# Performance work log

Measured on AMD Instinct MI355X. Metric: run time of the kernel, lower is better.

## Reference

```python
import jax, jax.numpy as jnp
import numpy as np

B, C, P, H, W = 64, 2048, 4, 14, 14
HID = C * P // 2  # 4096
S = H * W         # 196


def setup_inputs() -> dict:
    key = jax.random.key(0)
    k1, k2, k3, k4, k5 = jax.random.split(key, 5)
    x = jax.random.normal(k1, (B, C, H, W), dtype=jnp.float32)
    w1 = jax.random.normal(k2, (HID, C), dtype=jnp.float32) * 0.02
    b1 = jnp.zeros((HID,), dtype=jnp.float32)
    w2 = jax.random.normal(k3, (C * P, HID), dtype=jnp.float32) * 0.02
    b2 = jnp.zeros((C * P,), dtype=jnp.float32)
    return {"x": x, "w1": w1, "b1": b1, "w2": w2, "b2": b2}


def reference(x, w1, b1, w2, b2):
    # SE-style gating: global average pool -> fc1 -> sigmoid -> fc2 -> sigmoid
    g = x.mean(axis=(2, 3))                                  # [B, C]
    h = jax.nn.sigmoid(g @ w1.T + b1)                        # [B, HID]
    w = jax.nn.sigmoid(h @ w2.T + b2).reshape(B, P, C)       # grouping_result [B, P, C]
    # Weighted feature: mean over channels of w[b,p,c] * x[b,c,s].
    # Original materializes [B,P,C,196] then AdaptiveAvgPool3d over C;
    # mathematically this is a batched matmul divided by C.
    xs = x.reshape(B, C, S)                                  # [B, C, 196]
    feat = jnp.einsum('bpc,bcs->bps', w, xs) / C             # [B, P, 196]
    return (w, feat.reshape(B, P, H, W))
```

## Files before the change

kernel.cpp:

```cpp
#include <hip/hip_runtime.h>
#include <cstdint>
#include <cstddef>

typedef __attribute__((ext_vector_type(4))) float  f32x4;
typedef __attribute__((ext_vector_type(8))) short  short8;

__device__ __forceinline__ short f2bf(float f) {
  unsigned u = __float_as_uint(f);
  u += 0x7FFF + ((u >> 16) & 1);
  return (short)(u >> 16);
}
__device__ __forceinline__ float sigmoidf(float x) {
  return 1.0f / (1.0f + __expf(-x));
}

__global__ __launch_bounds__(256) void pool_kernel(const float* __restrict__ x,
                                                   short* __restrict__ g) {
  __shared__ float sums[784];
  const int tid = threadIdx.x;
  const f32x4* base = (const f32x4*)(x + (size_t)blockIdx.x * (16 * 196));
#pragma unroll
  for (int it = 0; it < 4; ++it) {
    int i = it * 256 + tid;
    if (it < 3 || tid < 16) {
      f32x4 v = base[i];
      sums[i] = v[0] + v[1] + v[2] + v[3];
    }
  }
  __syncthreads();
  if (tid < 16) {
    float s = 0.f;
#pragma unroll
    for (int j = 0; j < 49; ++j) s += sums[tid * 49 + j];
    g[blockIdx.x * 16 + tid] = f2bf(s * (1.0f / 196.0f));
  }
}

template<int N, int K, int WAVES, bool OUT_BF16, bool ZERO_FEAT>
__device__ __forceinline__ void gemm_body(const short* __restrict__ A,
                                          const float* __restrict__ B,
                                          const float* __restrict__ bias,
                                          void* __restrict__ outp,
                                          float* __restrict__ zbuf,
                                          float* __restrict__ red) {
  constexpr int KW = K / WAVES;
  constexpr int NK = KW / 32;
  constexpr int NT = WAVES * 64;
  const int n0  = blockIdx.x * 16;
  const int tid = threadIdx.x;
  const int l   = tid & 63;
  const int wv  = tid >> 6;
  const int kw0 = wv * KW;

  if constexpr (ZERO_FEAT) {
    if (tid < 98) zbuf[blockIdx.x * 98 + tid] = 0.f;
  }

  const int ko = (l >> 4) * 8;
  const float* Bp = B + (size_t)(n0 + (l & 15)) * K + kw0 + ko;
  const short* Ap = A + (size_t)(l & 15) * K + kw0 + ko;

  f32x4 acc0 = {}, acc1 = {}, acc2 = {}, acc3 = {};

  f32x4 bc0 = *(const f32x4*)(Bp);
  f32x4 bc1 = *(const f32x4*)(Bp + 4);
  short8 ac0 = *(const short8*)(Ap);
  short8 ac1 = *(const short8*)(Ap + 16 * K);
  short8 ac2 = *(const short8*)(Ap + 32 * K);
  short8 ac3 = *(const short8*)(Ap + 48 * K);

  for (int t = 0; t < NK; ++t) {
    f32x4 bn0 = {}, bn1 = {};
    short8 an0 = {}, an1 = {}, an2 = {}, an3 = {};
    if (t + 1 < NK) {
      const float* bp = Bp + (t + 1) * 32;
      const short* ap = Ap + (t + 1) * 32;
      bn0 = *(const f32x4*)(bp);
      bn1 = *(const f32x4*)(bp + 4);
      an0 = *(const short8*)(ap);
      an1 = *(const short8*)(ap + 16 * K);
      an2 = *(const short8*)(ap + 32 * K);
      an3 = *(const short8*)(ap + 48 * K);
    }
    short8 bb;
    bb[0] = f2bf(bc0[0]); bb[1] = f2bf(bc0[1]); bb[2] = f2bf(bc0[2]); bb[3] = f2bf(bc0[3]);
    bb[4] = f2bf(bc1[0]); bb[5] = f2bf(bc1[1]); bb[6] = f2bf(bc1[2]); bb[7] = f2bf(bc1[3]);
    acc0 = __builtin_amdgcn_mfma_f32_16x16x32_bf16(ac0, bb, acc0, 0, 0, 0);
    acc1 = __builtin_amdgcn_mfma_f32_16x16x32_bf16(ac1, bb, acc1, 0, 0, 0);
    acc2 = __builtin_amdgcn_mfma_f32_16x16x32_bf16(ac2, bb, acc2, 0, 0, 0);
    acc3 = __builtin_amdgcn_mfma_f32_16x16x32_bf16(ac3, bb, acc3, 0, 0, 0);
    bc0 = bn0; bc1 = bn1;
    ac0 = an0; ac1 = an1; ac2 = an2; ac3 = an3;
  }

  {
    float* rw = red + wv * 1024;
    const int mb = (l >> 4) << 2;
    const int nn = l & 15;
#pragma unroll
    for (int r = 0; r < 4; ++r) rw[(0  + mb + r) * 16 + nn] = acc0[r];
#pragma unroll
    for (int r = 0; r < 4; ++r) rw[(16 + mb + r) * 16 + nn] = acc1[r];
#pragma unroll
    for (int r = 0; r < 4; ++r) rw[(32 + mb + r) * 16 + nn] = acc2[r];
#pragma unroll
    for (int r = 0; r < 4; ++r) rw[(48 + mb + r) * 16 + nn] = acc3[r];
  }
  __syncthreads();

#pragma unroll
  for (int i = tid; i < 1024; i += NT) {
    float s = 0.f;
#pragma unroll
    for (int w = 0; w < WAVES; ++w) s += red[w * 1024 + i];
    int m  = i >> 4;
    int nn = n0 + (i & 15);
    s = sigmoidf(s + bias[nn]);
    if constexpr (OUT_BF16) ((short*)outp)[(size_t)m * N + nn] = f2bf(s);
    else                    ((float*)outp)[(size_t)m * N + nn] = s;
  }
}

__global__ __launch_bounds__(1024, 4) void gemm1_kernel(const short* __restrict__ A,
                                                        const float* __restrict__ B,
                                                        const float* __restrict__ bias,
                                                        short* __restrict__ outp) {
  __shared__ float red[16 * 1024];
  gemm_body<4096, 2048, 16, true, false>(A, B, bias, outp, nullptr, red);
}

__global__ __launch_bounds__(512, 4) void gemm2_kernel(const short* __restrict__ A,
                                                       const float* __restrict__ B,
                                                       const float* __restrict__ bias,
                                                       float* __restrict__ outp,
                                                       float* __restrict__ zbuf) {
  __shared__ float red[8 * 1024];
  gemm_body<8192, 4096, 8, false, true>(A, B, bias, outp, zbuf, red);
}

__global__ __launch_bounds__(256) void einsum_kernel(const float* __restrict__ x,
                                                     const float* __restrict__ wg,
                                                     float* __restrict__ feat) {
  const int b   = blockIdx.x >> 4;
  const int cc  = blockIdx.x & 15;
  const int tid = threadIdx.x;
  if (tid >= 196) return;
  const float* wp = wg + (size_t)b * 8192 + cc * 128;
  const float* xp = x + (size_t)b * 2048 * 196 + (size_t)cc * 128 * 196 + tid;
  float a0 = 0.f, a1 = 0.f, a2 = 0.f, a3 = 0.f;
#pragma unroll 8
  for (int c = 0; c < 128; ++c) {
    float xv = xp[(size_t)c * 196];
    a0 = __builtin_fmaf(wp[c],        xv, a0);
    a1 = __builtin_fmaf(wp[2048 + c], xv, a1);
    a2 = __builtin_fmaf(wp[4096 + c], xv, a2);
    a3 = __builtin_fmaf(wp[6144 + c], xv, a3);
  }
  const float invC = 1.0f / 2048.0f;
  atomicAdd(feat + (b * 4 + 0) * 196 + tid, a0 * invC);
  atomicAdd(feat + (b * 4 + 1) * 196 + tid, a1 * invC);
  atomicAdd(feat + (b * 4 + 2) * 196 + tid, a2 * invC);
  atomicAdd(feat + (b * 4 + 3) * 196 + tid, a3 * invC);
}

extern "C" void kernel_launch(void* const* d_in, const int* in_sizes, int n_in,
                              void* d_out, int out_size, void* d_ws, size_t ws_size,
                              hipStream_t stream) {
  const float* x  = (const float*)d_in[0];
  const float* w1 = (const float*)d_in[1];
  const float* b1 = (const float*)d_in[2];
  const float* w2 = (const float*)d_in[3];
  const float* b2 = (const float*)d_in[4];
  float* out = (float*)d_out;

  short* g_bf = (short*)d_ws;
  short* h_bf = g_bf + 64 * 2048;

  float* wout = out;
  float* feat = out + 524288;

  pool_kernel<<<8192, 256, 0, stream>>>(x, g_bf);

  gemm1_kernel<<<4096 / 16, 1024, 0, stream>>>(g_bf, w1, b1, h_bf);

  gemm2_kernel<<<8192 / 16, 512, 0, stream>>>(h_bf, w2, b2, wout, feat);

  einsum_kernel<<<64 * 16, 256, 0, stream>>>(x, wout, feat);
}
```

Baseline: 100.4 us.

## Vectorize einsum loads, drop A-prefetch in GEMM, raise gemm2 occupancy bound

The einsum kernel now has 49 threads per block, each loading four contiguous spatial values as a float4 and keeping four-wide accumulators per group. Block size falls from 256 to 64 threads. The GEMM loop no longer software-prefetches the bf16 A operand and instead loads it at the start of each iteration, which frees registers. gemm2's launch bound rises to 6 blocks per CU. f2bf now calls the HIP library conversion. Together these aim to cut per-element load overhead and register pressure, but they risk exposing A-load latency and leaving lanes idle in einsum waves.

```diff
diff --git a/kernel.cpp b/kernel.cpp
--- a/kernel.cpp
+++ b/kernel.cpp
@@ -1,4 +1,5 @@
 #include <hip/hip_runtime.h>
+#include <hip/hip_bf16.h>
 #include <cstdint>
 #include <cstddef>
 
@@ -6,9 +7,8 @@
 typedef __attribute__((ext_vector_type(8))) short  short8;
 
 __device__ __forceinline__ short f2bf(float f) {
-  unsigned u = __float_as_uint(f);
-  u += 0x7FFF + ((u >> 16) & 1);
-  return (short)(u >> 16);
+  __hip_bfloat16 h = __float2bfloat16(f);
+  return *reinterpret_cast<short*>(&h);
 }
 __device__ __forceinline__ float sigmoidf(float x) {
   return 1.0f / (1.0f + __expf(-x));
@@ -64,24 +64,19 @@
 
   f32x4 bc0 = *(const f32x4*)(Bp);
   f32x4 bc1 = *(const f32x4*)(Bp + 4);
-  short8 ac0 = *(const short8*)(Ap);
-  short8 ac1 = *(const short8*)(Ap + 16 * K);
-  short8 ac2 = *(const short8*)(Ap + 32 * K);
-  short8 ac3 = *(const short8*)(Ap + 48 * K);
 
   for (int t = 0; t < NK; ++t) {
     f32x4 bn0 = {}, bn1 = {};
-    short8 an0 = {}, an1 = {}, an2 = {}, an3 = {};
     if (t + 1 < NK) {
       const float* bp = Bp + (t + 1) * 32;
-      const short* ap = Ap + (t + 1) * 32;
       bn0 = *(const f32x4*)(bp);
       bn1 = *(const f32x4*)(bp + 4);
-      an0 = *(const short8*)(ap);
-      an1 = *(const short8*)(ap + 16 * K);
-      an2 = *(const short8*)(ap + 32 * K);
-      an3 = *(const short8*)(ap + 48 * K);
     }
+    const short* ap = Ap + t * 32;
+    short8 ac0 = *(const short8*)(ap);
+    short8 ac1 = *(const short8*)(ap + 16 * K);
+    short8 ac2 = *(const short8*)(ap + 32 * K);
+    short8 ac3 = *(const short8*)(ap + 48 * K);
     short8 bb;
     bb[0] = f2bf(bc0[0]); bb[1] = f2bf(bc0[1]); bb[2] = f2bf(bc0[2]); bb[3] = f2bf(bc0[3]);
     bb[4] = f2bf(bc1[0]); bb[5] = f2bf(bc1[1]); bb[6] = f2bf(bc1[2]); bb[7] = f2bf(bc1[3]);
@@ -90,7 +85,6 @@
     acc2 = __builtin_amdgcn_mfma_f32_16x16x32_bf16(ac2, bb, acc2, 0, 0, 0);
     acc3 = __builtin_amdgcn_mfma_f32_16x16x32_bf16(ac3, bb, acc3, 0, 0, 0);
     bc0 = bn0; bc1 = bn1;
-    ac0 = an0; ac1 = an1; ac2 = an2; ac3 = an3;
   }
 
   {
@@ -129,7 +123,7 @@
   gemm_body<4096, 2048, 16, true, false>(A, B, bias, outp, nullptr, red);
 }
 
-__global__ __launch_bounds__(512, 4) void gemm2_kernel(const short* __restrict__ A,
+__global__ __launch_bounds__(512, 6) void gemm2_kernel(const short* __restrict__ A,
                                                        const float* __restrict__ B,
                                                        const float* __restrict__ bias,
                                                        float* __restrict__ outp,
@@ -138,29 +132,37 @@
   gemm_body<8192, 4096, 8, false, true>(A, B, bias, outp, zbuf, red);
 }
 
-__global__ __launch_bounds__(256) void einsum_kernel(const float* __restrict__ x,
-                                                     const float* __restrict__ wg,
-                                                     float* __restrict__ feat) {
-  const int b   = blockIdx.x >> 4;
-  const int cc  = blockIdx.x & 15;
-  const int tid = threadIdx.x;
-  if (tid >= 196) return;
+__global__ __launch_bounds__(64) void einsum_kernel(const float* __restrict__ x,
+                                                    const float* __restrict__ wg,
+                                                    float* __restrict__ feat) {
+  const int b  = blockIdx.x >> 4;
+  const int cc = blockIdx.x & 15;
+  const int t  = threadIdx.x;
+  if (t >= 49) return;
   const float* wp = wg + (size_t)b * 8192 + cc * 128;
-  const float* xp = x + (size_t)b * 2048 * 196 + (size_t)cc * 128 * 196 + tid;
-  float a0 = 0.f, a1 = 0.f, a2 = 0.f, a3 = 0.f;
+  const float* xp = x + (size_t)b * 2048 * 196 + (size_t)cc * 128 * 196 + 4 * t;
+  f32x4 a0 = {}, a1 = {}, a2 = {}, a3 = {};
 #pragma unroll 8
   for (int c = 0; c < 128; ++c) {
-    float xv = xp[(size_t)c * 196];
-    a0 = __builtin_fmaf(wp[c],        xv, a0);
-    a1 = __builtin_fmaf(wp[2048 + c], xv, a1);
-    a2 = __builtin_fmaf(wp[4096 + c], xv, a2);
-    a3 = __builtin_fmaf(wp[6144 + c], xv, a3);
+    f32x4 xv = *(const f32x4*)(xp + (size_t)c * 196);
+    float w0 = wp[c], w1 = wp[2048 + c], w2 = wp[4096 + c], w3 = wp[6144 + c];
+#pragma unroll
+    for (int j = 0; j < 4; ++j) {
+      a0[j] = __builtin_fmaf(w0, xv[j], a0[j]);
+      a1[j] = __builtin_fmaf(w1, xv[j], a1[j]);
+      a2[j] = __builtin_fmaf(w2, xv[j], a2[j]);
+      a3[j] = __builtin_fmaf(w3, xv[j], a3[j]);
+    }
   }
   const float invC = 1.0f / 2048.0f;
-  atomicAdd(feat + (b * 4 + 0) * 196 + tid, a0 * invC);
-  atomicAdd(feat + (b * 4 + 1) * 196 + tid, a1 * invC);
-  atomicAdd(feat + (b * 4 + 2) * 196 + tid, a2 * invC);
-  atomicAdd(feat + (b * 4 + 3) * 196 + tid, a3 * invC);
+  float* fb = feat + (size_t)b * 4 * 196 + 4 * t;
+#pragma unroll
+  for (int j = 0; j < 4; ++j) {
+    atomicAdd(fb + 0 * 196 + j, a0[j] * invC);
+    atomicAdd(fb + 1 * 196 + j, a1[j] * invC);
+    atomicAdd(fb + 2 * 196 + j, a2[j] * invC);
+    atomicAdd(fb + 3 * 196 + j, a3[j] * invC);
+  }
 }
 
 extern "C" void kernel_launch(void* const* d_in, const int* in_sizes, int n_in,
@@ -185,5 +187,5 @@
 
   gemm2_kernel<<<8192 / 16, 512, 0, stream>>>(h_bf, w2, b2, wout, feat);
 
-  einsum_kernel<<<64 * 16, 256, 0, stream>>>(x, wout, feat);
+  einsum_kernel<<<64 * 16, 64, 0, stream>>>(x, wout, feat);
 }
```

After: 106.6 us. +6.2%, slower.
